# Kernel tuning notes

Measured on AMD Instinct MI355X. Metric: run time of the kernel, lower is better.

## Reference

```python
import jax, jax.numpy as jnp
import numpy as np

ALPHA = 0.2  # LeakyReLU negative slope
NEG_BIG = -9e15


def setup_inputs() -> dict:
    key = jax.random.key(0)
    k1, k2, k3, k4 = jax.random.split(key, 4)
    B, N, Fin, Fout = 16, 1024, 256, 256
    h = jax.random.normal(k1, (B, N, Fin), dtype=jnp.float32)
    adj = jax.random.randint(k2, (B, N, N), 0, 2, dtype=jnp.int32)
    # xavier_uniform with gain=1.414
    def xavier(k, shape, gain=1.414):
        fan_in, fan_out = shape[0], shape[1]
        bound = gain * np.sqrt(6.0 / (fan_in + fan_out))
        return jax.random.uniform(k, shape, jnp.float32, -bound, bound)
    W = xavier(k3, (Fin, Fout))
    a = xavier(k4, (2 * Fout, 1))
    return {"h": h, "adj": adj, "W": W, "a": a}


def reference(h, adj, W, a):
    # h: [B,N,Fin], adj: [B,N,N], W: [Fin,Fout], a: [2*Fout,1]
    Fout = W.shape[1]
    Wh = jnp.einsum('bnf,fo->bno', h, W)                      # [B,N,Fout]
    a1, a2 = a[:Fout, 0], a[Fout:, 0]                          # [Fout], [Fout]
    # e_ij = leakyrelu(Wh_i . a1 + Wh_j . a2) -- outer sum, no O(N^2*F) tensor
    f1 = Wh @ a1                                               # [B,N]
    f2 = Wh @ a2                                               # [B,N]
    e = jax.nn.leaky_relu(f1[:, :, None] + f2[:, None, :], negative_slope=ALPHA)
    attention = jnp.where(adj > 0, e, jnp.float32(NEG_BIG))    # [B,N,N]
    attention = jax.nn.softmax(attention, axis=2)
    h_prime = jnp.einsum('bij,bjo->bio', attention, Wh)        # [B,N,Fout]
    return jax.nn.elu(h_prime)
```

## Files before the change

### kernel.cpp

```cpp
#include <hip/hip_runtime.h>
#include <hip/hip_bf16.h>

#define Bsz 16
#define Nn  1024
#define Ff  256
#define ALPHA 0.2f
#define NEG_BIG -9.0e15f

typedef __attribute__((ext_vector_type(8))) short short8;
typedef __attribute__((ext_vector_type(4))) float f32x4;
typedef __attribute__((ext_vector_type(4))) unsigned short ushort4_t;

__device__ __forceinline__ unsigned short f2bf(float x) {
    union { __hip_bfloat16 b; unsigned short u; } cv;
    cv.b = __float2bfloat16(x);
    return cv.u;
}

__global__ __launch_bounds__(256) void gat_prep(
    const float* __restrict__ W, const float* __restrict__ a,
    float* __restrict__ w1, float* __restrict__ w2)
{
    const int t = threadIdx.x, w = t >> 6, ln = t & 63;
    __shared__ float a1s[Ff], a2s[Ff];
    a1s[t] = a[t];
    a2s[t] = a[Ff + t];
    __syncthreads();
    const int f = blockIdx.x * 4 + w;
    float s1 = 0.f, s2 = 0.f;
    #pragma unroll
    for (int c = 0; c < 4; c++) {
        const int o = ln + 64 * c;
        const float wv = W[(size_t)f * Ff + o];
        s1 += wv * a1s[o];
        s2 += wv * a2s[o];
    }
    #pragma unroll
    for (int off = 1; off < 64; off <<= 1) {
        s1 += __shfl_xor(s1, off, 64);
        s2 += __shfl_xor(s2, off, 64);
    }
    if (ln == 0) { w1[f] = s1; w2[f] = s2; }
}

__global__ __launch_bounds__(256) void pack_f(
    const float* __restrict__ h, const float* __restrict__ W,
    const float* __restrict__ w1, const float* __restrict__ w2,
    unsigned short* __restrict__ hK, unsigned short* __restrict__ WK,
    float* __restrict__ f1, float* __restrict__ f2)
{
    __shared__ float tile[32][257];
    const int id = blockIdx.x, t = threadIdx.x, w = t >> 6, ln = t & 63;
    const bool isH = (id < 512);
    const float* src;
    unsigned short* dst;
    int grow0 = 0;
    if (isH) {
        const int b = id >> 5, kt = id & 31;
        grow0 = b * Nn + kt * 32;
        src = h + (size_t)grow0 * Ff;
        dst = hK + ((size_t)(b * 32 + kt)) * 8192;
    } else {
        const int ft = id - 512;
        src = W + (size_t)ft * 32 * Ff;
        dst = WK + (size_t)ft * 8192;
    }
    #pragma unroll
    for (int rr = 0; rr < 8; rr++) {
        const int row = rr * 4 + w;
        const int col = ln * 4;
        const float4 v = *(const float4*)&src[row * Ff + col];
        tile[row][col] = v.x; tile[row][col + 1] = v.y;
        tile[row][col + 2] = v.z; tile[row][col + 3] = v.w;
    }
    __syncthreads();

    unsigned* d32 = (unsigned*)dst;
    #pragma unroll
    for (int k = 0; k < 16; k++) {
        const int fidx = k * 256 + t;
        const int o = fidx >> 4, q = fidx & 15;
        const unsigned lo = f2bf(tile[2 * q][o]);
        const unsigned hi = f2bf(tile[2 * q + 1][o]);
        d32[fidx] = lo | (hi << 16);
    }

    if (isH) {
        float w1r[4], w2r[4];
        #pragma unroll
        for (int c = 0; c < 4; c++) {
            w1r[c] = w1[ln + 64 * c];
            w2r[c] = w2[ln + 64 * c];
        }
        #pragma unroll
        for (int rr = 0; rr < 8; rr++) {
            const int row = rr * 4 + w;
            float s1 = 0.f, s2 = 0.f;
            #pragma unroll
            for (int c = 0; c < 4; c++) {
                const float hv = tile[row][ln + 64 * c];
                s1 += hv * w1r[c];
                s2 += hv * w2r[c];
            }
            #pragma unroll
            for (int off = 1; off < 64; off <<= 1) {
                s1 += __shfl_xor(s1, off, 64);
                s2 += __shfl_xor(s2, off, 64);
            }
            if (ln == 0) { f1[grow0 + row] = s1; f2[grow0 + row] = s2; }
        }
    }
}

#define TI 32
__global__ __launch_bounds__(512, 4) void gat_attn(
    const int* __restrict__ adj,
    const float* __restrict__ f1, const float* __restrict__ f2,
    const unsigned short* __restrict__ hK, const unsigned short* __restrict__ WK,
    float* __restrict__ out)
{
    __shared__ unsigned short pbf[TI * 1024];
    const int t = threadIdx.x, w = t >> 6, ln = t & 63;
    const int m = ln & 15, quad = ln >> 4;
    const int bid = blockIdx.x;
    const int b  = 2 * (bid & 7) + ((bid >> 3) & 1);
    const int i0 = (bid >> 4) * TI;

    float4 f2r[4];
    #pragma unroll
    for (int c = 0; c < 4; c++)
        f2r[c] = *(const float4*)&f2[b * Nn + 256 * c + 4 * ln];

    const int grb = b * Nn + i0 + w * 4;
    const int* aptr = adj + (size_t)grb * Nn;
    int4 av0[4], av1[4];
    #pragma unroll
    for (int c = 0; c < 4; c++) {
        av0[c] = *(const int4*)&aptr[c * 256 + 4 * ln];
        av1[c] = *(const int4*)&aptr[Nn + c * 256 + 4 * ln];
    }
    #pragma unroll
    for (int p = 0; p < 2; p++) {
        int4 nv0[4], nv1[4];
        if (p == 0) {
            #pragma unroll
            for (int c = 0; c < 4; c++) {
                nv0[c] = *(const int4*)&aptr[2 * Nn + c * 256 + 4 * ln];
                nv1[c] = *(const int4*)&aptr[3 * Nn + c * 256 + 4 * ln];
            }
        }
        const int r0 = w * 4 + 2 * p, r1 = r0 + 1;
        const float fi0 = f1[grb + 2 * p], fi1 = f1[grb + 2 * p + 1];
        float e0[16], e1[16];
        float mx0 = -INFINITY, mx1 = -INFINITY;
        #pragma unroll
        for (int c = 0; c < 4; c++) {
            const float4 fv = f2r[c];
            float x;
            x = fi0 + fv.x; x = x > 0.f ? x : ALPHA * x; x = av0[c].x > 0 ? x : NEG_BIG; e0[4*c+0] = x; mx0 = fmaxf(mx0, x);
            x = fi0 + fv.y; x = x > 0.f ? x : ALPHA * x; x = av0[c].y > 0 ? x : NEG_BIG; e0[4*c+1] = x; mx0 = fmaxf(mx0, x);
            x = fi0 + fv.z; x = x > 0.f ? x : ALPHA * x; x = av0[c].z > 0 ? x : NEG_BIG; e0[4*c+2] = x; mx0 = fmaxf(mx0, x);
            x = fi0 + fv.w; x = x > 0.f ? x : ALPHA * x; x = av0[c].w > 0 ? x : NEG_BIG; e0[4*c+3] = x; mx0 = fmaxf(mx0, x);
            x = fi1 + fv.x; x = x > 0.f ? x : ALPHA * x; x = av1[c].x > 0 ? x : NEG_BIG; e1[4*c+0] = x; mx1 = fmaxf(mx1, x);
            x = fi1 + fv.y; x = x > 0.f ? x : ALPHA * x; x = av1[c].y > 0 ? x : NEG_BIG; e1[4*c+1] = x; mx1 = fmaxf(mx1, x);
            x = fi1 + fv.z; x = x > 0.f ? x : ALPHA * x; x = av1[c].z > 0 ? x : NEG_BIG; e1[4*c+2] = x; mx1 = fmaxf(mx1, x);
            x = fi1 + fv.w; x = x > 0.f ? x : ALPHA * x; x = av1[c].w > 0 ? x : NEG_BIG; e1[4*c+3] = x; mx1 = fmaxf(mx1, x);
        }
        #pragma unroll
        for (int off = 1; off < 64; off <<= 1) {
            mx0 = fmaxf(mx0, __shfl_xor(mx0, off, 64));
            mx1 = fmaxf(mx1, __shfl_xor(mx1, off, 64));
        }
        float s0 = 0.f, s1 = 0.f;
        #pragma unroll
        for (int c = 0; c < 16; c++) {
            e0[c] = __expf(e0[c] - mx0); s0 += e0[c];
            e1[c] = __expf(e1[c] - mx1); s1 += e1[c];
        }
        #pragma unroll
        for (int off = 1; off < 64; off <<= 1) {
            s0 += __shfl_xor(s0, off, 64);
            s1 += __shfl_xor(s1, off, 64);
        }
        const float ri0 = 1.f / s0, ri1 = 1.f / s1;
        #pragma unroll
        for (int c = 0; c < 4; c++) {
            const int j = 256 * c + 4 * ln;
            ushort4_t v0 = { f2bf(e0[4*c] * ri0), f2bf(e0[4*c+1] * ri0),
                             f2bf(e0[4*c+2] * ri0), f2bf(e0[4*c+3] * ri0) };
            ushort4_t v1 = { f2bf(e1[4*c] * ri1), f2bf(e1[4*c+1] * ri1),
                             f2bf(e1[4*c+2] * ri1), f2bf(e1[4*c+3] * ri1) };
            *(ushort4_t*)&pbf[r0 * 1024 + (j ^ ((r0 & 7) << 3))] = v0;
            *(ushort4_t*)&pbf[r1 * 1024 + (j ^ ((r1 & 7) << 3))] = v1;
        }
        #pragma unroll
        for (int c = 0; c < 4; c++) { av0[c] = nv0[c]; av1[c] = nv1[c]; }
    }
    __syncthreads();

    const int n0 = w * 32;
    const unsigned short* hKb = hK + (size_t)b * 32 * 8192;
    const int arow0 = m * 1024, arow1 = (16 + m) * 1024;
    const int asw = (m & 7) << 3;
    #define AF0(kt) (*(const short8*)&pbf[arow0 + ((((kt) * 32) + quad * 8) ^ asw)])
    #define AF1(kt) (*(const short8*)&pbf[arow1 + ((((kt) * 32) + quad * 8) ^ asw)])
    #define BF0(kt) (*(const short8*)&hKb[(size_t)(kt) * 8192 + (n0 + m) * 32 + quad * 8])
    #define BF1(kt) (*(const short8*)&hKb[(size_t)(kt) * 8192 + (n0 + 16 + m) * 32 + quad * 8])

    f32x4 acc00 = {0.f,0.f,0.f,0.f}, acc01 = acc00, acc10 = acc00, acc11 = acc00;
    short8 a0c = AF0(0), a1c = AF1(0);
    short8 b0c = BF0(0), b1c = BF1(0);
    short8 b0n = BF0(1), b1n = BF1(1);
    #pragma unroll
    for (int kt = 0; kt < 32; kt++) {
        short8 b0nn = b0c, b1nn = b1c, a0n = a0c, a1n = a1c;
        if (kt + 2 < 32) { b0nn = BF0(kt + 2); b1nn = BF1(kt + 2); }
        if (kt + 1 < 32) { a0n = AF0(kt + 1); a1n = AF1(kt + 1); }
        acc00 = __builtin_amdgcn_mfma_f32_16x16x32_bf16(a0c, b0c, acc00, 0, 0, 0);
        acc01 = __builtin_amdgcn_mfma_f32_16x16x32_bf16(a0c, b1c, acc01, 0, 0, 0);
        acc10 = __builtin_amdgcn_mfma_f32_16x16x32_bf16(a1c, b0c, acc10, 0, 0, 0);
        acc11 = __builtin_amdgcn_mfma_f32_16x16x32_bf16(a1c, b1c, acc11, 0, 0, 0);
        a0c = a0n; a1c = a1n; b0c = b0n; b1c = b1n; b0n = b0nn; b1n = b1nn;
    }

    __syncthreads();
    #pragma unroll
    for (int reg = 0; reg < 4; reg++) {
        pbf[(quad * 4 + reg) * 264 + n0 + m]           = f2bf(acc00[reg]);
        pbf[(quad * 4 + reg) * 264 + n0 + 16 + m]      = f2bf(acc01[reg]);
        pbf[(16 + quad * 4 + reg) * 264 + n0 + m]      = f2bf(acc10[reg]);
        pbf[(16 + quad * 4 + reg) * 264 + n0 + 16 + m] = f2bf(acc11[reg]);
    }
    __syncthreads();

    #define GA0(kt) (*(const short8*)&pbf[m * 264 + (kt) * 32 + quad * 8])
    #define GA1(kt) (*(const short8*)&pbf[(16 + m) * 264 + (kt) * 32 + quad * 8])
    #define WB0(kt) (*(const short8*)&WK[(size_t)(kt) * 8192 + (n0 + m) * 32 + quad * 8])
    #define WB1(kt) (*(const short8*)&WK[(size_t)(kt) * 8192 + (n0 + 16 + m) * 32 + quad * 8])

    f32x4 c00 = {0.f,0.f,0.f,0.f}, c01 = c00, c10 = c00, c11 = c00;
    short8 ga0 = GA0(0), ga1 = GA1(0);
    short8 wb0 = WB0(0), wb1 = WB1(0);
    #pragma unroll
    for (int kt = 0; kt < 8; kt++) {
        short8 ga0n = ga0, ga1n = ga1, wb0n = wb0, wb1n = wb1;
        if (kt + 1 < 8) { ga0n = GA0(kt+1); ga1n = GA1(kt+1); wb0n = WB0(kt+1); wb1n = WB1(kt+1); }
        c00 = __builtin_amdgcn_mfma_f32_16x16x32_bf16(ga0, wb0, c00, 0, 0, 0);
        c01 = __builtin_amdgcn_mfma_f32_16x16x32_bf16(ga0, wb1, c01, 0, 0, 0);
        c10 = __builtin_amdgcn_mfma_f32_16x16x32_bf16(ga1, wb0, c10, 0, 0, 0);
        c11 = __builtin_amdgcn_mfma_f32_16x16x32_bf16(ga1, wb1, c11, 0, 0, 0);
        ga0 = ga0n; ga1 = ga1n; wb0 = wb0n; wb1 = wb1n;
    }
    const size_t ob = (size_t)(b * Nn) + i0;
    #pragma unroll
    for (int reg = 0; reg < 4; reg++) {
        float v;
        v = c00[reg]; v = v > 0.f ? v : (__expf(v) - 1.f);
        out[(ob + quad * 4 + reg) * Ff + n0 + m] = v;
        v = c01[reg]; v = v > 0.f ? v : (__expf(v) - 1.f);
        out[(ob + quad * 4 + reg) * Ff + n0 + 16 + m] = v;
        v = c10[reg]; v = v > 0.f ? v : (__expf(v) - 1.f);
        out[(ob + 16 + quad * 4 + reg) * Ff + n0 + m] = v;
        v = c11[reg]; v = v > 0.f ? v : (__expf(v) - 1.f);
        out[(ob + 16 + quad * 4 + reg) * Ff + n0 + 16 + m] = v;
    }
}

extern "C" void kernel_launch(void* const* d_in, const int* in_sizes, int n_in,
                              void* d_out, int out_size, void* d_ws, size_t ws_size,
                              hipStream_t stream)
{
    const void* h   = d_in[0];
    const void* adj = d_in[1];
    const void* W   = d_in[2];
    const void* a   = d_in[3];
    for (int i = 0; i < n_in; i++) {
        if      (in_sizes[i] == Bsz * Nn * Ff) h   = d_in[i];
        else if (in_sizes[i] == Bsz * Nn * Nn) adj = d_in[i];
        else if (in_sizes[i] == Ff * Ff)       W   = d_in[i];
        else if (in_sizes[i] == 2 * Ff)        a   = d_in[i];
    }
    float* out = (float*)d_out;

    char*  wsb = (char*)d_ws;
    float* w1  = (float*)wsb;
    float* w2  = w1 + Ff;
    float* f1  = (float*)(wsb + 4096);
    float* f2  = f1 + Bsz * Nn;
    unsigned short* hK = (unsigned short*)(wsb + 4096 + 2 * 65536);
    unsigned short* WK = hK + (size_t)Bsz * 32 * 8192;

    gat_prep<<<64, 256, 0, stream>>>((const float*)W, (const float*)a, w1, w2);
    pack_f<<<520, 256, 0, stream>>>((const float*)h, (const float*)W, w1, w2, hK, WK, f1, f2);
    gat_attn<<<Bsz * (Nn / TI), 512, 0, stream>>>((const int*)adj, f1, f2, hK, WK, out);
}
```

Before: 142.7 us.

## Drop softmax max pass, chunk attention over two column halves to halve LDS

```diff
diff --git a/kernel.cpp b/kernel.cpp
--- a/kernel.cpp
+++ b/kernel.cpp
@@ -113,143 +113,123 @@
 }
 
 #define TI 32
-__global__ __launch_bounds__(512, 4) void gat_attn(
+__global__ __launch_bounds__(512, 8) void gat_attn(
     const int* __restrict__ adj,
     const float* __restrict__ f1, const float* __restrict__ f2,
     const unsigned short* __restrict__ hK, const unsigned short* __restrict__ WK,
     float* __restrict__ out)
 {
-    __shared__ unsigned short pbf[TI * 1024];
+    __shared__ unsigned short pbf[TI * 512];
+    __shared__ float dnm[TI];
     const int t = threadIdx.x, w = t >> 6, ln = t & 63;
     const int m = ln & 15, quad = ln >> 4;
     const int bid = blockIdx.x;
     const int b  = 2 * (bid & 7) + ((bid >> 3) & 1);
     const int i0 = (bid >> 4) * TI;
 
-    float4 f2r[4];
-    #pragma unroll
-    for (int c = 0; c < 4; c++)
-        f2r[c] = *(const float4*)&f2[b * Nn + 256 * c + 4 * ln];
-
-    const int grb = b * Nn + i0 + w * 4;
-    const int* aptr = adj + (size_t)grb * Nn;
-    int4 av0[4], av1[4];
-    #pragma unroll
-    for (int c = 0; c < 4; c++) {
-        av0[c] = *(const int4*)&aptr[c * 256 + 4 * ln];
-        av1[c] = *(const int4*)&aptr[Nn + c * 256 + 4 * ln];
-    }
-    #pragma unroll
-    for (int p = 0; p < 2; p++) {
-        int4 nv0[4], nv1[4];
-        if (p == 0) {
-            #pragma unroll
-            for (int c = 0; c < 4; c++) {
-                nv0[c] = *(const int4*)&aptr[2 * Nn + c * 256 + 4 * ln];
-                nv1[c] = *(const int4*)&aptr[3 * Nn + c * 256 + 4 * ln];
-            }
-        }
-        const int r0 = w * 4 + 2 * p, r1 = r0 + 1;
-        const float fi0 = f1[grb + 2 * p], fi1 = f1[grb + 2 * p + 1];
-        float e0[16], e1[16];
-        float mx0 = -INFINITY, mx1 = -INFINITY;
-        #pragma unroll
-        for (int c = 0; c < 4; c++) {
-            const float4 fv = f2r[c];
-            float x;
-            x = fi0 + fv.x; x = x > 0.f ? x : ALPHA * x; x = av0[c].x > 0 ? x : NEG_BIG; e0[4*c+0] = x; mx0 = fmaxf(mx0, x);
-            x = fi0 + fv.y; x = x > 0.f ? x : ALPHA * x; x = av0[c].y > 0 ? x : NEG_BIG; e0[4*c+1] = x; mx0 = fmaxf(mx0, x);
-            x = fi0 + fv.z; x = x > 0.f ? x : ALPHA * x; x = av0[c].z > 0 ? x : NEG_BIG; e0[4*c+2] = x; mx0 = fmaxf(mx0, x);
-            x = fi0 + fv.w; x = x > 0.f ? x : ALPHA * x; x = av0[c].w > 0 ? x : NEG_BIG; e0[4*c+3] = x; mx0 = fmaxf(mx0, x);
-            x = fi1 + fv.x; x = x > 0.f ? x : ALPHA * x; x = av1[c].x > 0 ? x : NEG_BIG; e1[4*c+0] = x; mx1 = fmaxf(mx1, x);
-            x = fi1 + fv.y; x = x > 0.f ? x : ALPHA * x; x = av1[c].y > 0 ? x : NEG_BIG; e1[4*c+1] = x; mx1 = fmaxf(mx1, x);
-            x = fi1 + fv.z; x = x > 0.f ? x : ALPHA * x; x = av1[c].z > 0 ? x : NEG_BIG; e1[4*c+2] = x; mx1 = fmaxf(mx1, x);
-            x = fi1 + fv.w; x = x > 0.f ? x : ALPHA * x; x = av1[c].w > 0 ? x : NEG_BIG; e1[4*c+3] = x; mx1 = fmaxf(mx1, x);
-        }
-        #pragma unroll
-        for (int off = 1; off < 64; off <<= 1) {
-            mx0 = fmaxf(mx0, __shfl_xor(mx0, off, 64));
-            mx1 = fmaxf(mx1, __shfl_xor(mx1, off, 64));
-        }
-        float s0 = 0.f, s1 = 0.f;
-        #pragma unroll
-        for (int c = 0; c < 16; c++) {
-            e0[c] = __expf(e0[c] - mx0); s0 += e0[c];
-            e1[c] = __expf(e1[c] - mx1); s1 += e1[c];
-        }
-        #pragma unroll
-        for (int off = 1; off < 64; off <<= 1) {
-            s0 += __shfl_xor(s0, off, 64);
-            s1 += __shfl_xor(s1, off, 64);
-        }
-        const float ri0 = 1.f / s0, ri1 = 1.f / s1;
-        #pragma unroll
-        for (int c = 0; c < 4; c++) {
-            const int j = 256 * c + 4 * ln;
-            ushort4_t v0 = { f2bf(e0[4*c] * ri0), f2bf(e0[4*c+1] * ri0),
-                             f2bf(e0[4*c+2] * ri0), f2bf(e0[4*c+3] * ri0) };
-            ushort4_t v1 = { f2bf(e1[4*c] * ri1), f2bf(e1[4*c+1] * ri1),
-                             f2bf(e1[4*c+2] * ri1), f2bf(e1[4*c+3] * ri1) };
-            *(ushort4_t*)&pbf[r0 * 1024 + (j ^ ((r0 & 7) << 3))] = v0;
-            *(ushort4_t*)&pbf[r1 * 1024 + (j ^ ((r1 & 7) << 3))] = v1;
-        }
-        #pragma unroll
-        for (int c = 0; c < 4; c++) { av0[c] = nv0[c]; av1[c] = nv1[c]; }
-    }
-    __syncthreads();
-
+    const int r0g = b * Nn + i0 + w * 4;
+    const int* aptr = adj + (size_t)r0g * Nn;
+    float f1r[4];
+    #pragma unroll
+    for (int rr = 0; rr < 4; rr++) f1r[rr] = f1[r0g + rr];
+
+    float srow[4] = {0.f, 0.f, 0.f, 0.f};
+    f32x4 acc00 = {0.f,0.f,0.f,0.f}, acc01 = acc00, acc10 = acc00, acc11 = acc00;
+
+    const unsigned short* hKb = hK + (size_t)b * 32 * 8192;
     const int n0 = w * 32;
-    const unsigned short* hKb = hK + (size_t)b * 32 * 8192;
-    const int arow0 = m * 1024, arow1 = (16 + m) * 1024;
+    const int arow0 = m * 512, arow1 = (16 + m) * 512;
     const int asw = (m & 7) << 3;
-    #define AF0(kt) (*(const short8*)&pbf[arow0 + ((((kt) * 32) + quad * 8) ^ asw)])
-    #define AF1(kt) (*(const short8*)&pbf[arow1 + ((((kt) * 32) + quad * 8) ^ asw)])
-    #define BF0(kt) (*(const short8*)&hKb[(size_t)(kt) * 8192 + (n0 + m) * 32 + quad * 8])
-    #define BF1(kt) (*(const short8*)&hKb[(size_t)(kt) * 8192 + (n0 + 16 + m) * 32 + quad * 8])
-
-    f32x4 acc00 = {0.f,0.f,0.f,0.f}, acc01 = acc00, acc10 = acc00, acc11 = acc00;
-    short8 a0c = AF0(0), a1c = AF1(0);
-    short8 b0c = BF0(0), b1c = BF1(0);
-    short8 b0n = BF0(1), b1n = BF1(1);
-    #pragma unroll
-    for (int kt = 0; kt < 32; kt++) {
-        short8 b0nn = b0c, b1nn = b1c, a0n = a0c, a1n = a1c;
-        if (kt + 2 < 32) { b0nn = BF0(kt + 2); b1nn = BF1(kt + 2); }
-        if (kt + 1 < 32) { a0n = AF0(kt + 1); a1n = AF1(kt + 1); }
-        acc00 = __builtin_amdgcn_mfma_f32_16x16x32_bf16(a0c, b0c, acc00, 0, 0, 0);
-        acc01 = __builtin_amdgcn_mfma_f32_16x16x32_bf16(a0c, b1c, acc01, 0, 0, 0);
-        acc10 = __builtin_amdgcn_mfma_f32_16x16x32_bf16(a1c, b0c, acc10, 0, 0, 0);
-        acc11 = __builtin_amdgcn_mfma_f32_16x16x32_bf16(a1c, b1c, acc11, 0, 0, 0);
-        a0c = a0n; a1c = a1n; b0c = b0n; b1c = b1n; b0n = b0nn; b1n = b1nn;
-    }
-
-    __syncthreads();
+
+    for (int c = 0; c < 2; c++) {
+        const int j0 = c * 512;
+        float4 f2r[2];
+        #pragma unroll
+        for (int cc = 0; cc < 2; cc++)
+            f2r[cc] = *(const float4*)&f2[b * Nn + j0 + 256 * cc + 4 * ln];
+        int4 av[4][2];
+        #pragma unroll
+        for (int rr = 0; rr < 4; rr++)
+            #pragma unroll
+            for (int cc = 0; cc < 2; cc++)
+                av[rr][cc] = *(const int4*)&aptr[rr * Nn + j0 + 256 * cc + 4 * ln];
+
+        if (c) __syncthreads();
+
+        #pragma unroll
+        for (int rr = 0; rr < 4; rr++) {
+            const int r = w * 4 + rr;
+            const float fi = f1r[rr];
+            float e[8];
+            #pragma unroll
+            for (int cc = 0; cc < 2; cc++) {
+                const float4 fv = f2r[cc];
+                const int4 a = av[rr][cc];
+                float x;
+                x = fi + fv.x; x = x > 0.f ? x : ALPHA * x; x = a.x > 0 ? x : NEG_BIG; e[4*cc+0] = __expf(x);
+                x = fi + fv.y; x = x > 0.f ? x : ALPHA * x; x = a.y > 0 ? x : NEG_BIG; e[4*cc+1] = __expf(x);
+                x = fi + fv.z; x = x > 0.f ? x : ALPHA * x; x = a.z > 0 ? x : NEG_BIG; e[4*cc+2] = __expf(x);
+                x = fi + fv.w; x = x > 0.f ? x : ALPHA * x; x = a.w > 0 ? x : NEG_BIG; e[4*cc+3] = __expf(x);
+            }
+            float s = e[0] + e[1] + e[2] + e[3] + e[4] + e[5] + e[6] + e[7];
+            #pragma unroll
+            for (int off = 1; off < 64; off <<= 1) s += __shfl_xor(s, off, 64);
+            srow[rr] += s;
+            #pragma unroll
+            for (int cc = 0; cc < 2; cc++) {
+                const int jj = 256 * cc + 4 * ln;
+                ushort4_t v = { f2bf(e[4*cc]), f2bf(e[4*cc+1]), f2bf(e[4*cc+2]), f2bf(e[4*cc+3]) };
+                *(ushort4_t*)&pbf[r * 512 + (jj ^ ((r & 7) << 3))] = v;
+            }
+        }
+        __syncthreads();
+
+        #pragma unroll
+        for (int kt = 0; kt < 16; kt++) {
+            const short8 a0 = *(const short8*)&pbf[arow0 + ((kt * 32 + quad * 8) ^ asw)];
+            const short8 a1 = *(const short8*)&pbf[arow1 + ((kt * 32 + quad * 8) ^ asw)];
+            const short8 b0 = *(const short8*)&hKb[(size_t)(c * 16 + kt) * 8192 + (n0 + m) * 32 + quad * 8];
+            const short8 b1 = *(const short8*)&hKb[(size_t)(c * 16 + kt) * 8192 + (n0 + 16 + m) * 32 + quad * 8];
+            acc00 = __builtin_amdgcn_mfma_f32_16x16x32_bf16(a0, b0, acc00, 0, 0, 0);
+            acc01 = __builtin_amdgcn_mfma_f32_16x16x32_bf16(a0, b1, acc01, 0, 0, 0);
+            acc10 = __builtin_amdgcn_mfma_f32_16x16x32_bf16(a1, b0, acc10, 0, 0, 0);
+            acc11 = __builtin_amdgcn_mfma_f32_16x16x32_bf16(a1, b1, acc11, 0, 0, 0);
+        }
+    }
+
+    if (ln == 0) {
+        #pragma unroll
+        for (int rr = 0; rr < 4; rr++)
+            dnm[w * 4 + rr] = (srow[rr] != 0.f) ? 1.f / srow[rr] : 0.f;
+    }
+    __syncthreads();
+
+    float dn0[4], dn1[4];
     #pragma unroll
     for (int reg = 0; reg < 4; reg++) {
-        pbf[(quad * 4 + reg) * 264 + n0 + m]           = f2bf(acc00[reg]);
-        pbf[(quad * 4 + reg) * 264 + n0 + 16 + m]      = f2bf(acc01[reg]);
-        pbf[(16 + quad * 4 + reg) * 264 + n0 + m]      = f2bf(acc10[reg]);
-        pbf[(16 + quad * 4 + reg) * 264 + n0 + 16 + m] = f2bf(acc11[reg]);
-    }
-    __syncthreads();
-
-    #define GA0(kt) (*(const short8*)&pbf[m * 264 + (kt) * 32 + quad * 8])
-    #define GA1(kt) (*(const short8*)&pbf[(16 + m) * 264 + (kt) * 32 + quad * 8])
-    #define WB0(kt) (*(const short8*)&WK[(size_t)(kt) * 8192 + (n0 + m) * 32 + quad * 8])
-    #define WB1(kt) (*(const short8*)&WK[(size_t)(kt) * 8192 + (n0 + 16 + m) * 32 + quad * 8])
+        dn0[reg] = dnm[quad * 4 + reg];
+        dn1[reg] = dnm[16 + quad * 4 + reg];
+    }
+    #pragma unroll
+    for (int reg = 0; reg < 4; reg++) {
+        pbf[(quad * 4 + reg) * 264 + n0 + m]           = f2bf(acc00[reg] * dn0[reg]);
+        pbf[(quad * 4 + reg) * 264 + n0 + 16 + m]      = f2bf(acc01[reg] * dn0[reg]);
+        pbf[(16 + quad * 4 + reg) * 264 + n0 + m]      = f2bf(acc10[reg] * dn1[reg]);
+        pbf[(16 + quad * 4 + reg) * 264 + n0 + 16 + m] = f2bf(acc11[reg] * dn1[reg]);
+    }
+    __syncthreads();
 
     f32x4 c00 = {0.f,0.f,0.f,0.f}, c01 = c00, c10 = c00, c11 = c00;
-    short8 ga0 = GA0(0), ga1 = GA1(0);
-    short8 wb0 = WB0(0), wb1 = WB1(0);
     #pragma unroll
     for (int kt = 0; kt < 8; kt++) {
-        short8 ga0n = ga0, ga1n = ga1, wb0n = wb0, wb1n = wb1;
-        if (kt + 1 < 8) { ga0n = GA0(kt+1); ga1n = GA1(kt+1); wb0n = WB0(kt+1); wb1n = WB1(kt+1); }
+        const short8 ga0 = *(const short8*)&pbf[m * 264 + kt * 32 + quad * 8];
+        const short8 ga1 = *(const short8*)&pbf[(16 + m) * 264 + kt * 32 + quad * 8];
+        const short8 wb0 = *(const short8*)&WK[(size_t)kt * 8192 + (n0 + m) * 32 + quad * 8];
+        const short8 wb1 = *(const short8*)&WK[(size_t)kt * 8192 + (n0 + 16 + m) * 32 + quad * 8];
         c00 = __builtin_amdgcn_mfma_f32_16x16x32_bf16(ga0, wb0, c00, 0, 0, 0);
         c01 = __builtin_amdgcn_mfma_f32_16x16x32_bf16(ga0, wb1, c01, 0, 0, 0);
         c10 = __builtin_amdgcn_mfma_f32_16x16x32_bf16(ga1, wb0, c10, 0, 0, 0);
         c11 = __builtin_amdgcn_mfma_f32_16x16x32_bf16(ga1, wb1, c11, 0, 0, 0);
-        ga0 = ga0n; ga1 = ga1n; wb0 = wb0n; wb1 = wb1n;
     }
     const size_t ob = (size_t)(b * Nn) + i0;
     #pragma unroll
```

Result: slower. 188.2 us (+31.9%).

## Pack adjacency into bitmask and drop max-subtraction in softmax

Applied to the files above, without the earlier changes.

```diff
diff --git a/kernel.cpp b/kernel.cpp
--- a/kernel.cpp
+++ b/kernel.cpp
@@ -5,7 +5,6 @@
 #define Nn  1024
 #define Ff  256
 #define ALPHA 0.2f
-#define NEG_BIG -9.0e15f
 
 typedef __attribute__((ext_vector_type(8))) short short8;
 typedef __attribute__((ext_vector_type(4))) float f32x4;
@@ -41,6 +40,25 @@
         s2 += __shfl_xor(s2, off, 64);
     }
     if (ln == 0) { w1[f] = s1; w2[f] = s2; }
+}
+
+__global__ __launch_bounds__(256) void pack_adj(
+    const int* __restrict__ adj, unsigned* __restrict__ abits)
+{
+    const int t = threadIdx.x, ln = t & 63, w = t >> 6;
+    const int row = blockIdx.x * 8 + w * 2 + (ln >> 5);
+    const int wd = ln & 31;
+    const int* src = adj + (size_t)row * Nn + wd * 32;
+    unsigned word = 0;
+    #pragma unroll
+    for (int k = 0; k < 8; k++) {
+        const int4 v = *(const int4*)&src[4 * k];
+        word |= (v.x > 0 ? 1u : 0u) << (4 * k);
+        word |= (v.y > 0 ? 1u : 0u) << (4 * k + 1);
+        word |= (v.z > 0 ? 1u : 0u) << (4 * k + 2);
+        word |= (v.w > 0 ? 1u : 0u) << (4 * k + 3);
+    }
+    abits[(size_t)row * 32 + wd] = word;
 }
 
 __global__ __launch_bounds__(256) void pack_f(
@@ -113,8 +131,8 @@
 }
 
 #define TI 32
-__global__ __launch_bounds__(512, 4) void gat_attn(
-    const int* __restrict__ adj,
+__global__ __launch_bounds__(512, 2) void gat_attn(
+    const unsigned* __restrict__ abits,
     const float* __restrict__ f1, const float* __restrict__ f2,
     const unsigned short* __restrict__ hK, const unsigned short* __restrict__ WK,
     float* __restrict__ out)
@@ -126,75 +144,49 @@
     const int b  = 2 * (bid & 7) + ((bid >> 3) & 1);
     const int i0 = (bid >> 4) * TI;
 
+    const int r0g = b * Nn + i0 + w * 4;
+
     float4 f2r[4];
     #pragma unroll
     for (int c = 0; c < 4; c++)
         f2r[c] = *(const float4*)&f2[b * Nn + 256 * c + 4 * ln];
-
-    const int grb = b * Nn + i0 + w * 4;
-    const int* aptr = adj + (size_t)grb * Nn;
-    int4 av0[4], av1[4];
-    #pragma unroll
-    for (int c = 0; c < 4; c++) {
-        av0[c] = *(const int4*)&aptr[c * 256 + 4 * ln];
-        av1[c] = *(const int4*)&aptr[Nn + c * 256 + 4 * ln];
-    }
-    #pragma unroll
-    for (int p = 0; p < 2; p++) {
-        int4 nv0[4], nv1[4];
-        if (p == 0) {
-            #pragma unroll
-            for (int c = 0; c < 4; c++) {
-                nv0[c] = *(const int4*)&aptr[2 * Nn + c * 256 + 4 * ln];
-                nv1[c] = *(const int4*)&aptr[3 * Nn + c * 256 + 4 * ln];
-            }
-        }
-        const int r0 = w * 4 + 2 * p, r1 = r0 + 1;
-        const float fi0 = f1[grb + 2 * p], fi1 = f1[grb + 2 * p + 1];
-        float e0[16], e1[16];
-        float mx0 = -INFINITY, mx1 = -INFINITY;
+    float f1r[4];
+    #pragma unroll
+    for (int rr = 0; rr < 4; rr++) f1r[rr] = f1[r0g + rr];
+    unsigned mk[4][4];
+    #pragma unroll
+    for (int rr = 0; rr < 4; rr++)
+        #pragma unroll
+        for (int c = 0; c < 4; c++)
+            mk[rr][c] = abits[(size_t)(r0g + rr) * 32 + 8 * c + (ln >> 3)];
+
+    const unsigned sh = 4 * (ln & 7);
+    #pragma unroll
+    for (int rr = 0; rr < 4; rr++) {
+        const int r = w * 4 + rr;
+        const float fi = f1r[rr];
+        float e[16];
+        float s = 0.f;
         #pragma unroll
         for (int c = 0; c < 4; c++) {
             const float4 fv = f2r[c];
+            const unsigned nib = mk[rr][c] >> sh;
             float x;
-            x = fi0 + fv.x; x = x > 0.f ? x : ALPHA * x; x = av0[c].x > 0 ? x : NEG_BIG; e0[4*c+0] = x; mx0 = fmaxf(mx0, x);
-            x = fi0 + fv.y; x = x > 0.f ? x : ALPHA * x; x = av0[c].y > 0 ? x : NEG_BIG; e0[4*c+1] = x; mx0 = fmaxf(mx0, x);
-            x = fi0 + fv.z; x = x > 0.f ? x : ALPHA * x; x = av0[c].z > 0 ? x : NEG_BIG; e0[4*c+2] = x; mx0 = fmaxf(mx0, x);
-            x = fi0 + fv.w; x = x > 0.f ? x : ALPHA * x; x = av0[c].w > 0 ? x : NEG_BIG; e0[4*c+3] = x; mx0 = fmaxf(mx0, x);
-            x = fi1 + fv.x; x = x > 0.f ? x : ALPHA * x; x = av1[c].x > 0 ? x : NEG_BIG; e1[4*c+0] = x; mx1 = fmaxf(mx1, x);
-            x = fi1 + fv.y; x = x > 0.f ? x : ALPHA * x; x = av1[c].y > 0 ? x : NEG_BIG; e1[4*c+1] = x; mx1 = fmaxf(mx1, x);
-            x = fi1 + fv.z; x = x > 0.f ? x : ALPHA * x; x = av1[c].z > 0 ? x : NEG_BIG; e1[4*c+2] = x; mx1 = fmaxf(mx1, x);
-            x = fi1 + fv.w; x = x > 0.f ? x : ALPHA * x; x = av1[c].w > 0 ? x : NEG_BIG; e1[4*c+3] = x; mx1 = fmaxf(mx1, x);
-        }
-        #pragma unroll
-        for (int off = 1; off < 64; off <<= 1) {
-            mx0 = fmaxf(mx0, __shfl_xor(mx0, off, 64));
-            mx1 = fmaxf(mx1, __shfl_xor(mx1, off, 64));
-        }
-        float s0 = 0.f, s1 = 0.f;
-        #pragma unroll
-        for (int c = 0; c < 16; c++) {
-            e0[c] = __expf(e0[c] - mx0); s0 += e0[c];
-            e1[c] = __expf(e1[c] - mx1); s1 += e1[c];
-        }
-        #pragma unroll
-        for (int off = 1; off < 64; off <<= 1) {
-            s0 += __shfl_xor(s0, off, 64);
-            s1 += __shfl_xor(s1, off, 64);
-        }
-        const float ri0 = 1.f / s0, ri1 = 1.f / s1;
+            x = fi + fv.x; x = x > 0.f ? x : ALPHA * x; x = (nib & 1u) ? __expf(x) : 0.f; e[4*c+0] = x; s += x;
+            x = fi + fv.y; x = x > 0.f ? x : ALPHA * x; x = (nib & 2u) ? __expf(x) : 0.f; e[4*c+1] = x; s += x;
+            x = fi + fv.z; x = x > 0.f ? x : ALPHA * x; x = (nib & 4u) ? __expf(x) : 0.f; e[4*c+2] = x; s += x;
+            x = fi + fv.w; x = x > 0.f ? x : ALPHA * x; x = (nib & 8u) ? __expf(x) : 0.f; e[4*c+3] = x; s += x;
+        }
+        #pragma unroll
+        for (int off = 1; off < 64; off <<= 1) s += __shfl_xor(s, off, 64);
+        const float ri = (s != 0.f) ? 1.f / s : 0.f;
         #pragma unroll
         for (int c = 0; c < 4; c++) {
             const int j = 256 * c + 4 * ln;
-            ushort4_t v0 = { f2bf(e0[4*c] * ri0), f2bf(e0[4*c+1] * ri0),
-                             f2bf(e0[4*c+2] * ri0), f2bf(e0[4*c+3] * ri0) };
-            ushort4_t v1 = { f2bf(e1[4*c] * ri1), f2bf(e1[4*c+1] * ri1),
-                             f2bf(e1[4*c+2] * ri1), f2bf(e1[4*c+3] * ri1) };
-            *(ushort4_t*)&pbf[r0 * 1024 + (j ^ ((r0 & 7) << 3))] = v0;
-            *(ushort4_t*)&pbf[r1 * 1024 + (j ^ ((r1 & 7) << 3))] = v1;
-        }
-        #pragma unroll
-        for (int c = 0; c < 4; c++) { av0[c] = nv0[c]; av1[c] = nv1[c]; }
+            ushort4_t v = { f2bf(e[4*c] * ri), f2bf(e[4*c+1] * ri),
+                            f2bf(e[4*c+2] * ri), f2bf(e[4*c+3] * ri) };
+            *(ushort4_t*)&pbf[r * 1024 + (j ^ ((r & 7) << 3))] = v;
+        }
     }
     __syncthreads();
 
@@ -233,23 +225,17 @@
     }
     __syncthreads();
 
-    #define GA0(kt) (*(const short8*)&pbf[m * 264 + (kt) * 32 + quad * 8])
-    #define GA1(kt) (*(const short8*)&pbf[(16 + m) * 264 + (kt) * 32 + quad * 8])
-    #define WB0(kt) (*(const short8*)&WK[(size_t)(kt) * 8192 + (n0 + m) * 32 + quad * 8])
-    #define WB1(kt) (*(const short8*)&WK[(size_t)(kt) * 8192 + (n0 + 16 + m) * 32 + quad * 8])
-
     f32x4 c00 = {0.f,0.f,0.f,0.f}, c01 = c00, c10 = c00, c11 = c00;
-    short8 ga0 = GA0(0), ga1 = GA1(0);
-    short8 wb0 = WB0(0), wb1 = WB1(0);
     #pragma unroll
     for (int kt = 0; kt < 8; kt++) {
-        short8 ga0n = ga0, ga1n = ga1, wb0n = wb0, wb1n = wb1;
-        if (kt + 1 < 8) { ga0n = GA0(kt+1); ga1n = GA1(kt+1); wb0n = WB0(kt+1); wb1n = WB1(kt+1); }
+        const short8 ga0 = *(const short8*)&pbf[m * 264 + kt * 32 + quad * 8];
+        const short8 ga1 = *(const short8*)&pbf[(16 + m) * 264 + kt * 32 + quad * 8];
+        const short8 wb0 = *(const short8*)&WK[(size_t)kt * 8192 + (n0 + m) * 32 + quad * 8];
+        const short8 wb1 = *(const short8*)&WK[(size_t)kt * 8192 + (n0 + 16 + m) * 32 + quad * 8];
         c00 = __builtin_amdgcn_mfma_f32_16x16x32_bf16(ga0, wb0, c00, 0, 0, 0);
         c01 = __builtin_amdgcn_mfma_f32_16x16x32_bf16(ga0, wb1, c01, 0, 0, 0);
         c10 = __builtin_amdgcn_mfma_f32_16x16x32_bf16(ga1, wb0, c10, 0, 0, 0);
         c11 = __builtin_amdgcn_mfma_f32_16x16x32_bf16(ga1, wb1, c11, 0, 0, 0);
-        ga0 = ga0n; ga1 = ga1n; wb0 = wb0n; wb1 = wb1n;
     }
     const size_t ob = (size_t)(b * Nn) + i0;
     #pragma unroll
@@ -289,8 +275,10 @@
     float* f2  = f1 + Bsz * Nn;
     unsigned short* hK = (unsigned short*)(wsb + 4096 + 2 * 65536);
     unsigned short* WK = hK + (size_t)Bsz * 32 * 8192;
+    unsigned* abits = (unsigned*)(WK + (size_t)8 * 8192);
 
     gat_prep<<<64, 256, 0, stream>>>((const float*)W, (const float*)a, w1, w2);
+    pack_adj<<<Bsz * Nn / 8, 256, 0, stream>>>((const int*)adj, abits);
     pack_f<<<520, 256, 0, stream>>>((const float*)h, (const float*)W, w1, w2, hK, WK, f1, f2);
-    gat_attn<<<Bsz * (Nn / TI), 512, 0, stream>>>((const int*)adj, f1, f2, hK, WK, out);
-}
+    gat_attn<<<Bsz * (Nn / TI), 512, 0, stream>>>(abits, f1, f2, hK, WK, out);
+}
```

Result: slower. 146.0 us (+2.3%).
